# Optimization experiments

Measured on AMD Instinct MI355X. Metric: run time of the kernel, lower is better.

The kernel has to match this reference:

```python
import jax, jax.numpy as jnp
import numpy as np
import math

B, T, C, H = 4, 2048, 1024, 16
HS = C // H
EPS = 1e-5


def layernorm(x, g, b):
    mu = jnp.mean(x, axis=-1, keepdims=True)
    var = jnp.var(x, axis=-1, keepdims=True)
    return (x - mu) * jax.lax.rsqrt(var + EPS) * g + b


def setup_inputs() -> dict:
    key = jax.random.key(0)
    ks = jax.random.split(key, 7)
    rn = lambda k, s: jax.random.normal(k, s, dtype=jnp.float32) * 0.02
    return {
        "x": jax.random.normal(ks[0], (B, T, C), dtype=jnp.float32),
        "mask": jnp.tril(jnp.ones((T, T), dtype=jnp.int32)),  # causal tril buffer
        "wq": rn(ks[1], (H, HS, C)),  # stacked per-head Linear weights [out,in]
        "wk": rn(ks[2], (H, HS, C)),
        "wv": rn(ks[3], (H, HS, C)),
        "ln1_g": jnp.ones((C,), jnp.float32),
        "ln1_b": jnp.zeros((C,), jnp.float32),
        "ln2_g": jnp.ones((C,), jnp.float32),
        "ln2_b": jnp.zeros((C,), jnp.float32),
        "w1": rn(ks[4], (4 * C, C)),
        "b1": jnp.zeros((4 * C,), jnp.float32),
        "w2": rn(ks[5], (C, 4 * C)),
        "b2": jnp.zeros((C,), jnp.float32),
    }


def reference(x, mask, wq, wk, wv, ln1_g, ln1_b, ln2_g, ln2_b, w1, b1, w2, b2):
    Bx, Tx, Cx = x.shape
    h = layernorm(x, ln1_g, ln1_b)
    # per-head projections, batched over heads: [B,H,T,HS]
    q = jnp.einsum('btc,hdc->bhtd', h, wq)
    k = jnp.einsum('btc,hdc->bhtd', h, wk)
    v = jnp.einsum('btc,hdc->bhtd', h, wv)
    scores = jnp.einsum('bhtd,bhsd->bhts', q, k) * (1.0 / math.sqrt(HS))
    scores = jnp.where(mask[None, None, :Tx, :Tx] == 0, -jnp.inf, scores)
    w = jax.nn.softmax(scores, axis=-1)
    attn = jnp.einsum('bhts,bhsd->bhtd', w, v)  # [B,H,T,HS]
    attn = attn.transpose(0, 2, 1, 3).reshape(Bx, Tx, Cx)  # concat heads
    x = x + attn
    h2 = layernorm(x, ln2_g, ln2_b)
    ff = jax.nn.silu(h2 @ w1.T + b1) @ w2.T + b2  # dropout = identity (eval)
    return x + ff
```

## Files before the change

### kernel.cpp

```cpp
#include <hip/hip_runtime.h>
#include <stdint.h>

#define Bb 4
#define Tt 2048
#define Cc 1024
#define Hh 16
#define HSs 64

typedef __attribute__((ext_vector_type(8))) __bf16 bf16x8;
typedef __attribute__((ext_vector_type(4))) float f32x4;

__device__ __forceinline__ ushort f2bf(float f){
  union { float f; uint u; } c; c.f = f;
  return (ushort)((c.u + 0x8000u) >> 16);
}
__device__ __forceinline__ float bf2f(ushort u){
  union { uint u; float f; } c; c.u = ((uint)u) << 16; return c.f;
}

__device__ __forceinline__ void gload16(const void* g, void* l){
  __builtin_amdgcn_global_load_lds(
      (__attribute__((address_space(1))) void*)(g),
      (__attribute__((address_space(3))) void*)(l), 16, 0, 0);
}

__global__ __launch_bounds__(256) void cast_all_kernel(
    const float* __restrict__ wq, const float* __restrict__ wk,
    const float* __restrict__ wv, const float* __restrict__ w1,
    const float* __restrict__ w2, ushort* __restrict__ out){
  int i = (blockIdx.x * 256 + threadIdx.x) * 4;
  const float* src; int off;
  if      (i <  1048576){ src = wq; off = i; }
  else if (i <  2097152){ src = wk; off = i - 1048576; }
  else if (i <  3145728){ src = wv; off = i - 2097152; }
  else if (i <  7340032){ src = w1; off = i - 3145728; }
  else                  { src = w2; off = i - 7340032; }
  float4 v = *(const float4*)(src + off);
  ushort4 o; o.x = f2bf(v.x); o.y = f2bf(v.y); o.z = f2bf(v.z); o.w = f2bf(v.w);
  *(ushort4*)(out + i) = o;
}

__global__ __launch_bounds__(256) void add_p1_kernel(float* __restrict__ out,
                                                     const ushort* __restrict__ p1b){
  for (int it = 0; it < 4; ++it){
    size_t i = ((size_t)it * 2048 * 256 + blockIdx.x * 256 + threadIdx.x) * 4;
    float4 o = *(const float4*)(out + i);
    ushort4 p = *(const ushort4*)(p1b + i);
    o.x += bf2f(p.x); o.y += bf2f(p.y); o.z += bf2f(p.z); o.w += bf2f(p.w);
    *(float4*)(out + i) = o;
  }
}

__global__ __launch_bounds__(256) void ln1_kernel(const float* __restrict__ x,
    const float* __restrict__ gw, const float* __restrict__ bw,
    ushort* __restrict__ hout){
  int row = blockIdx.x, tid = threadIdx.x;
  size_t base = (size_t)row * Cc + tid * 4;
  float4 xv = *(const float4*)(x + base);
  float s  = xv.x + xv.y + xv.z + xv.w;
  float ss = xv.x*xv.x + xv.y*xv.y + xv.z*xv.z + xv.w*xv.w;
  #pragma unroll
  for (int off = 1; off < 64; off <<= 1){ s += __shfl_xor(s, off); ss += __shfl_xor(ss, off); }
  __shared__ float red[8];
  int wid = tid >> 6, lane = tid & 63;
  if (lane == 0){ red[wid] = s; red[4 + wid] = ss; }
  __syncthreads();
  s  = red[0] + red[1] + red[2] + red[3];
  ss = red[4] + red[5] + red[6] + red[7];
  float mu = s * (1.0f / Cc);
  float rstd = rsqrtf(ss * (1.0f / Cc) - mu * mu + 1e-5f);
  float4 gv = *(const float4*)(gw + tid * 4);
  float4 bv = *(const float4*)(bw + tid * 4);
  ushort4 o;
  o.x = f2bf((xv.x - mu) * rstd * gv.x + bv.x);
  o.y = f2bf((xv.y - mu) * rstd * gv.y + bv.y);
  o.z = f2bf((xv.z - mu) * rstd * gv.z + bv.z);
  o.w = f2bf((xv.w - mu) * rstd * gv.w + bv.w);
  *(ushort4*)(hout + base) = o;
}

__global__ __launch_bounds__(256) void ln2_kernel(const float* __restrict__ x,
    const ushort* __restrict__ attnb,
    const float* __restrict__ gw, const float* __restrict__ bw,
    float* __restrict__ x2, ushort* __restrict__ hout){
  int row = blockIdx.x, tid = threadIdx.x;
  size_t base = (size_t)row * Cc + tid * 4;
  float4 xv = *(const float4*)(x + base);
  ushort4 av = *(const ushort4*)(attnb + base);
  xv.x += bf2f(av.x); xv.y += bf2f(av.y); xv.z += bf2f(av.z); xv.w += bf2f(av.w);
  *(float4*)(x2 + base) = xv;
  float s  = xv.x + xv.y + xv.z + xv.w;
  float ss = xv.x*xv.x + xv.y*xv.y + xv.z*xv.z + xv.w*xv.w;
  #pragma unroll
  for (int off = 1; off < 64; off <<= 1){ s += __shfl_xor(s, off); ss += __shfl_xor(ss, off); }
  __shared__ float red[8];
  int wid = tid >> 6, lane = tid & 63;
  if (lane == 0){ red[wid] = s; red[4 + wid] = ss; }
  __syncthreads();
  s  = red[0] + red[1] + red[2] + red[3];
  ss = red[4] + red[5] + red[6] + red[7];
  float mu = s * (1.0f / Cc);
  float rstd = rsqrtf(ss * (1.0f / Cc) - mu * mu + 1e-5f);
  float4 gv = *(const float4*)(gw + tid * 4);
  float4 bv = *(const float4*)(bw + tid * 4);
  ushort4 o;
  o.x = f2bf((xv.x - mu) * rstd * gv.x + bv.x);
  o.y = f2bf((xv.y - mu) * rstd * gv.y + bv.y);
  o.z = f2bf((xv.z - mu) * rstd * gv.z + bv.z);
  o.w = f2bf((xv.w - mu) * rstd * gv.w + bv.w);
  *(ushort4*)(hout + base) = o;
}

#define MFMA_QUAD(SI, QI, BQ) \
  { \
    _Pragma("unroll") \
    for (int mi = 0; mi < 4; ++mi){ \
      acc[(SI)*4+mi][(QI)*2+0] = __builtin_amdgcn_mfma_f32_16x16x32_bf16(af[mi][0], BQ[0][0], acc[(SI)*4+mi][(QI)*2+0], 0,0,0); \
      acc[(SI)*4+mi][(QI)*2+0] = __builtin_amdgcn_mfma_f32_16x16x32_bf16(af[mi][1], BQ[0][1], acc[(SI)*4+mi][(QI)*2+0], 0,0,0); \
      acc[(SI)*4+mi][(QI)*2+1] = __builtin_amdgcn_mfma_f32_16x16x32_bf16(af[mi][0], BQ[1][0], acc[(SI)*4+mi][(QI)*2+1], 0,0,0); \
      acc[(SI)*4+mi][(QI)*2+1] = __builtin_amdgcn_mfma_f32_16x16x32_bf16(af[mi][1], BQ[1][1], acc[(SI)*4+mi][(QI)*2+1], 0,0,0); \
    } \
  }

#define PH_SYNC_PRE()  { __builtin_amdgcn_sched_barrier(0); __builtin_amdgcn_s_barrier(); \
                         asm volatile("s_waitcnt lgkmcnt(0)" ::: "memory"); \
                         __builtin_amdgcn_sched_barrier(0); __builtin_amdgcn_s_setprio(1); }
#define PH_SYNC_POST() { __builtin_amdgcn_s_setprio(0); __builtin_amdgcn_sched_barrier(0); \
                         __builtin_amdgcn_s_barrier(); }

template<int MODE>
__device__ __forceinline__ void gemm256_body(
    const ushort* __restrict__ A, const ushort* __restrict__ Bw,
    int N, int K, int ldO,
    ushort* __restrict__ obf, float* __restrict__ of32,
    ushort* __restrict__ p1b, const float* __restrict__ bias)
{
  __shared__ __align__(16) ushort lds[2][2][2][128 * 64];
  int tid = threadIdx.x, lane = tid & 63, wid = tid >> 6;
  int wm = wid >> 2, wn = wid & 3;
  int c = lane & 15, g = lane >> 4;

  int nwg = gridDim.x, bid = blockIdx.x;
  int wgid = (bid & 7) * (nwg >> 3) + (bid >> 3);
  int m0, n0, koff = 0;
  if (MODE == 3){
    int split = wgid >> 7, rem = wgid & 127;
    m0 = (rem >> 2) << 8; n0 = (rem & 3) << 8; koff = split << 11;
  } else {
    int nTn = N >> 8;
    m0 = (wgid / nTn) << 8; n0 = (wgid % nTn) << 8;
  }

  const ushort* Ag = A  + (size_t)m0 * K + koff;
  const ushort* Bg = Bw + (size_t)n0 * K + koff;

  auto stage = [&](const ushort* gbase, int t, int ab, int h){
    #pragma unroll
    for (int j = 0; j < 2; ++j){
      int d = j * 8192 + wid * 1024 + lane * 16;
      int row = d >> 7;
      int colb = (d & 127) ^ ((row & 7) << 4);
      gload16((const char*)gbase + ((size_t)(h * 128 + row) * K + t * 64) * 2 + colb,
              (char*)&lds[t & 1][ab][h][0] + j * 8192 + wid * 1024);
    }
  };

  f32x4 acc[8][4] = {};
  bf16x8 af[4][2], bq0[2][2], bq1[2][2];
  int nt = (MODE == 3) ? (K >> 7) : (K >> 6);

  stage(Ag, 0, 0, 0); stage(Ag, 0, 0, 1);
  stage(Bg, 0, 1, 0); stage(Bg, 0, 1, 1);
  stage(Bg, 1, 1, 0); stage(Bg, 1, 1, 1);
  asm volatile("s_waitcnt vmcnt(4)" ::: "memory");
  __builtin_amdgcn_sched_barrier(0);
  __builtin_amdgcn_s_barrier();

  for (int t = 0; t < nt; ++t){
    const char* Abuf = (const char*)&lds[t & 1][0][wm][0];
    const char* Bbuf = (const char*)&lds[t & 1][1][wn >> 1][0];
    int brow0 = (wn & 1) * 64;

    #pragma unroll
    for (int mi = 0; mi < 4; ++mi){
      int row = mi * 16 + c, sw = (row & 7) << 4;
      af[mi][0] = *(const bf16x8*)(Abuf + row * 128 + ((g * 16) ^ sw));
      af[mi][1] = *(const bf16x8*)(Abuf + row * 128 + ((64 + g * 16) ^ sw));
    }
    #pragma unroll
    for (int nj = 0; nj < 2; ++nj){
      int row = brow0 + nj * 16 + c, sw = (row & 7) << 4;
      bq0[nj][0] = *(const bf16x8*)(Bbuf + row * 128 + ((g * 16) ^ sw));
      bq0[nj][1] = *(const bf16x8*)(Bbuf + row * 128 + ((64 + g * 16) ^ sw));
    }
    if (t + 1 < nt) stage(Ag, t + 1, 0, 0);
    PH_SYNC_PRE();
    MFMA_QUAD(0, 0, bq0);
    PH_SYNC_POST();

    #pragma unroll
    for (int nj = 0; nj < 2; ++nj){
      int row = brow0 + 32 + nj * 16 + c, sw = (row & 7) << 4;
      bq1[nj][0] = *(const bf16x8*)(Bbuf + row * 128 + ((g * 16) ^ sw));
      bq1[nj][1] = *(const bf16x8*)(Bbuf + row * 128 + ((64 + g * 16) ^ sw));
    }
    if (t + 1 < nt) stage(Ag, t + 1, 0, 1);
    PH_SYNC_PRE();
    MFMA_QUAD(0, 1, bq1);
    PH_SYNC_POST();

    #pragma unroll
    for (int mi = 0; mi < 4; ++mi){
      int row = 64 + mi * 16 + c, sw = (row & 7) << 4;
      af[mi][0] = *(const bf16x8*)(Abuf + row * 128 + ((g * 16) ^ sw));
      af[mi][1] = *(const bf16x8*)(Abuf + row * 128 + ((64 + g * 16) ^ sw));
    }
    if (t + 2 < nt) stage(Bg, t + 2, 1, 0);
    PH_SYNC_PRE();
    MFMA_QUAD(1, 0, bq0);
    PH_SYNC_POST();

    if (t + 2 < nt){
      stage(Bg, t + 2, 1, 1);
      asm volatile("s_waitcnt vmcnt(4)" ::: "memory");
    } else {
      asm volatile("s_waitcnt vmcnt(0)" ::: "memory");
    }
    __builtin_amdgcn_sched_barrier(0);
    __builtin_amdgcn_s_barrier();
    __builtin_amdgcn_s_setprio(1);
    MFMA_QUAD(1, 1, bq1);
    PH_SYNC_POST();
  }

  #pragma unroll
  for (int mi = 0; mi < 8; ++mi){
    #pragma unroll
    for (int ni = 0; ni < 4; ++ni){
      #pragma unroll
      for (int r = 0; r < 4; ++r){
        float v = acc[mi][ni][r];
        int m = m0 + wm * 128 + mi * 16 + g * 4 + r;
        int n = n0 + wn * 64 + ni * 16 + c;
        if (MODE == 0){
          int which = n >> 10;
          int nn = n & 1023;
          int b = m >> 11, t = m & (Tt - 1);
          int h = nn >> 6, d = nn & 63;
          float vv = (which == 0) ? v * 0.125f : v;
          size_t base = (size_t)which * (size_t)(Bb * Tt * Cc);
          size_t idx = (which == 2)
              ? ((((size_t)(b * Hh + h)) * HSs + d) * Tt + t)
              : ((((size_t)(b * Hh + h)) * Tt + t) * HSs + d);
          obf[base + idx] = f2bf(vv);
        } else if (MODE == 1){
          v += bias[n];
          float sv = v / (1.0f + __expf(-v));
          obf[(size_t)m * ldO + n] = f2bf(sv);
        } else {
          size_t idx = (size_t)m * N + n;
          if (koff == 0) of32[idx] = of32[idx] + v + bias[n];
          else           p1b[idx] = f2bf(v);
        }
      }
    }
  }
}

__global__ __launch_bounds__(512, 2) void gemm_qkv_kernel(
    const ushort* __restrict__ A, const ushort* __restrict__ Bw, int N, int K,
    ushort* __restrict__ obf){
  gemm256_body<0>(A, Bw, N, K, 0, obf, nullptr, nullptr, nullptr);
}
__global__ __launch_bounds__(512, 2) void gemm_ffn1_kernel(
    const ushort* __restrict__ A, const ushort* __restrict__ Bw, int N, int K, int ldO,
    ushort* __restrict__ obf, const float* __restrict__ bias){
  gemm256_body<1>(A, Bw, N, K, ldO, obf, nullptr, nullptr, bias);
}
__global__ __launch_bounds__(512, 2) void gemm_ffn2_kernel(
    const ushort* __restrict__ A, const ushort* __restrict__ Bw, int N, int K,
    float* __restrict__ of32, ushort* __restrict__ p1b, const float* __restrict__ bias){
  gemm256_body<3>(A, Bw, N, K, N, nullptr, of32, p1b, bias);
}

__global__ __launch_bounds__(256, 2) void attn_kernel(
    const ushort* __restrict__ q, const ushort* __restrict__ k,
    const ushort* __restrict__ vt, ushort* __restrict__ attnb)
{
  __shared__ __align__(16) ushort Ksm[4][64 * 64];
  __shared__ __align__(16) ushort Vsm[4][64 * 64];
  __shared__ __align__(16) ushort Pl[4][32 * 64];

  int bh  = blockIdx.y;
  int p   = blockIdx.x;
  int tid = threadIdx.x, wid = tid >> 6, lane = tid & 63;
  int g = lane >> 4, c = lane & 15;
  int qbA = 15 - p, qbB = p;
  int q0A = qbA * 128 + wid * 32;
  int q0B = qbB * 128 + wid * 32;
  const ushort* Qb = q  + (size_t)bh * Tt * HSs;
  const ushort* Kb = k  + (size_t)bh * Tt * HSs;
  const ushort* Vt = vt + (size_t)bh * HSs * Tt;
  char* Pw = (char*)&Pl[wid][0];

  auto stageKV = [&](int bsel, int s0){
    #pragma unroll
    for (int half = 0; half < 2; ++half){
      int i = wid + half * 4;
      int row = i * 8 + (lane >> 3);
      int col = ((lane & 7) ^ (row & 7)) * 8;
      gload16(Kb + (size_t)(s0 + row) * HSs + col, &Ksm[bsel][i * 512]);
      gload16(Vt + (size_t)row * Tt + s0 + col,    &Vsm[bsel][i * 512]);
    }
  };

  bf16x8 qfA[2][2], qfB[2][2];
  #pragma unroll
  for (int mi = 0; mi < 2; ++mi)
    #pragma unroll
    for (int ks = 0; ks < 2; ++ks){
      qfA[mi][ks] = *(const bf16x8*)(Qb + (size_t)(q0A + mi * 16 + c) * HSs + ks * 32 + g * 8);
      qfB[mi][ks] = *(const bf16x8*)(Qb + (size_t)(q0B + mi * 16 + c) * HSs + ks * 32 + g * 8);
    }

  f32x4 oA[2][4] = {}, oB[2][4] = {};
  float mA[2][4], lA[2][4], mB[2][4], lB[2][4];
  #pragma unroll
  for (int mi = 0; mi < 2; ++mi)
    #pragma unroll
    for (int r = 0; r < 4; ++r){
      mA[mi][r] = -1e30f; lA[mi][r] = 0.f;
      mB[mi][r] = -1e30f; lB[mi][r] = 0.f;
    }

  auto computeTile = [&](bf16x8 (&qf)[2][2], f32x4 (&o)[2][4],
                         float (&mrow)[2][4], float (&lpart)[2][4],
                         int q0w, int s0, const char* Kbuf, const char* Vbuf){
    f32x4 S[2][4] = {};
    bf16x8 kf[4][2];
    #pragma unroll
    for (int ni = 0; ni < 4; ++ni)
      #pragma unroll
      for (int ks = 0; ks < 2; ++ks)
        kf[ni][ks] = *(const bf16x8*)(Kbuf + (ni * 16 + c) * 128 + (((ks * 4 + g) ^ (c & 7)) << 4));
    #pragma unroll
    for (int mi = 0; mi < 2; ++mi)
      #pragma unroll
      for (int ni = 0; ni < 4; ++ni)
        #pragma unroll
        for (int ks = 0; ks < 2; ++ks)
          S[mi][ni] = __builtin_amdgcn_mfma_f32_16x16x32_bf16(qf[mi][ks], kf[ni][ks], S[mi][ni], 0, 0, 0);

    if (s0 + 63 > q0w){
      #pragma unroll
      for (int mi = 0; mi < 2; ++mi)
        #pragma unroll
        for (int ni = 0; ni < 4; ++ni)
          #pragma unroll
          for (int r = 0; r < 4; ++r){
            int tl = q0w + mi * 16 + g * 4 + r, sl = s0 + ni * 16 + c;
            if (sl > tl) S[mi][ni][r] = -1e30f;
          }
    }

    float lmax[2][4], worst = -1e30f;
    #pragma unroll
    for (int mi = 0; mi < 2; ++mi)
      #pragma unroll
      for (int r = 0; r < 4; ++r){
        float a0 = fmaxf(S[mi][0][r], S[mi][1][r]);
        float a1 = fmaxf(S[mi][2][r], S[mi][3][r]);
        lmax[mi][r] = fmaxf(a0, a1);
        worst = fmaxf(worst, lmax[mi][r] - mrow[mi][r]);
      }
    if (!__all(worst <= 8.0f)){
      #pragma unroll
      for (int mi = 0; mi < 2; ++mi)
        #pragma unroll
        for (int r = 0; r < 4; ++r){
          float mx = lmax[mi][r];
          mx = fmaxf(mx, __shfl_xor(mx, 1));
          mx = fmaxf(mx, __shfl_xor(mx, 2));
          mx = fmaxf(mx, __shfl_xor(mx, 4));
          mx = fmaxf(mx, __shfl_xor(mx, 8));
          float mnew  = fmaxf(mrow[mi][r], mx);
          float alpha = __expf(mrow[mi][r] - mnew);
          lpart[mi][r] *= alpha;
          #pragma unroll
          for (int dt = 0; dt < 4; ++dt) o[mi][dt][r] *= alpha;
          mrow[mi][r] = mnew;
        }
    }
    #pragma unroll
    for (int mi = 0; mi < 2; ++mi)
      #pragma unroll
      for (int r = 0; r < 4; ++r){
        int row = mi * 16 + g * 4 + r;
        float mb = mrow[mi][r] * 1.44269504f;
        float pp[4];
        #pragma unroll
        for (int ni = 0; ni < 4; ++ni){
          pp[ni] = exp2f(__builtin_fmaf(S[mi][ni][r], 1.44269504f, -mb));
          *(ushort*)(Pw + row * 128 + (((ni * 32 + 2 * c) ^ ((row & 7) << 4)))) = f2bf(pp[ni]);
        }
        lpart[mi][r] += (pp[0] + pp[1]) + (pp[2] + pp[3]);
      }

    bf16x8 vf[4][2];
    #pragma unroll
    for (int dt = 0; dt < 4; ++dt)
      #pragma unroll
      for (int ks = 0; ks < 2; ++ks)
        vf[dt][ks] = *(const bf16x8*)(Vbuf + (dt * 16 + c) * 128 + (((ks * 4 + g) ^ (c & 7)) << 4));
    #pragma unroll
    for (int mi = 0; mi < 2; ++mi){
      #pragma unroll
      for (int ks = 0; ks < 2; ++ks){
        bf16x8 pf = *(const bf16x8*)(Pw + (mi * 16 + c) * 128 + ((((ks * 4 + g) ^ (c & 7)) << 4)));
        #pragma unroll
        for (int dt = 0; dt < 4; ++dt)
          o[mi][dt] = __builtin_amdgcn_mfma_f32_16x16x32_bf16(pf, vf[dt][ks], o[mi][dt], 0, 0, 0);
      }
    }
  };

  int nchA = 2 * qbA + 2;

  stageKV(0, 0);
  stageKV(1, 64);

  for (int ch = 0; ch < nchA; ch += 2){
    bool staged = (ch + 2 < nchA);
    if (staged){
      stageKV((ch + 2) & 3, (ch + 2) * 64);
      stageKV((ch + 3) & 3, (ch + 3) * 64);
      asm volatile("s_waitcnt vmcnt(8)" ::: "memory");
    } else {
      asm volatile("s_waitcnt vmcnt(0)" ::: "memory");
    }
    __builtin_amdgcn_sched_barrier(0);
    __builtin_amdgcn_s_barrier();

    {
      int s0 = ch * 64;
      const char* Kbuf = (const char*)&Ksm[ch & 3][0];
      const char* Vbuf = (const char*)&Vsm[ch & 3][0];
      if (s0 <= q0A + 31) computeTile(qfA, oA, mA, lA, q0A, s0, Kbuf, Vbuf);
      if (s0 <= q0B + 31) computeTile(qfB, oB, mB, lB, q0B, s0, Kbuf, Vbuf);
    }
    {
      int s0 = (ch + 1) * 64;
      const char* Kbuf = (const char*)&Ksm[(ch + 1) & 3][0];
      const char* Vbuf = (const char*)&Vsm[(ch + 1) & 3][0];
      if (s0 <= q0A + 31) computeTile(qfA, oA, mA, lA, q0A, s0, Kbuf, Vbuf);
      if (s0 <= q0B + 31) computeTile(qfB, oB, mB, lB, q0B, s0, Kbuf, Vbuf);
    }

    __builtin_amdgcn_sched_barrier(0);
    __builtin_amdgcn_s_barrier();
  }

  int b = bh >> 4, h = bh & 15;
  #pragma unroll
  for (int mi = 0; mi < 2; ++mi)
    #pragma unroll
    for (int r = 0; r < 4; ++r){
      float la = lA[mi][r];
      la += __shfl_xor(la, 1); la += __shfl_xor(la, 2);
      la += __shfl_xor(la, 4); la += __shfl_xor(la, 8);
      float lia = 1.0f / la;
      float lb = lB[mi][r];
      lb += __shfl_xor(lb, 1); lb += __shfl_xor(lb, 2);
      lb += __shfl_xor(lb, 4); lb += __shfl_xor(lb, 8);
      float lib = 1.0f / lb;
      #pragma unroll
      for (int dt = 0; dt < 4; ++dt){
        int tA = q0A + mi * 16 + g * 4 + r;
        int tB = q0B + mi * 16 + g * 4 + r;
        attnb[((size_t)(b * Tt + tA)) * Cc + h * HSs + dt * 16 + c] = f2bf(oA[mi][dt][r] * lia);
        attnb[((size_t)(b * Tt + tB)) * Cc + h * HSs + dt * 16 + c] = f2bf(oB[mi][dt][r] * lib);
      }
    }
}

extern "C" void kernel_launch(void* const* d_in, const int* in_sizes, int n_in,
                              void* d_out, int out_size, void* d_ws, size_t ws_size,
                              hipStream_t stream) {
  (void)in_sizes; (void)n_in; (void)out_size; (void)ws_size;
  const float* x    = (const float*)d_in[0];
  const float* wq   = (const float*)d_in[2];
  const float* wk   = (const float*)d_in[3];
  const float* wv   = (const float*)d_in[4];
  const float* ln1g = (const float*)d_in[5];
  const float* ln1b = (const float*)d_in[6];
  const float* ln2g = (const float*)d_in[7];
  const float* ln2b = (const float*)d_in[8];
  const float* w1   = (const float*)d_in[9];
  const float* b1   = (const float*)d_in[10];
  const float* w2   = (const float*)d_in[11];
  const float* b2   = (const float*)d_in[12];
  float* out = (float*)d_out;

  char* ws = (char*)d_ws;
  const size_t SZ_ACT = (size_t)Bb * Tt * Cc * 2;
  ushort* h1    = (ushort*)(ws);
  ushort* qbuf  = (ushort*)(ws + SZ_ACT);
  ushort* kbuf  = (ushort*)(ws + 2 * SZ_ACT);
  ushort* vbuf  = (ushort*)(ws + 3 * SZ_ACT);
  ushort* attnb = (ushort*)(ws + 4 * SZ_ACT);
  ushort* h2    = (ushort*)(ws + 5 * SZ_ACT);
  ushort* h3    = (ushort*)(ws + 6 * SZ_ACT);
  ushort* p1b   = (ushort*)(ws + SZ_ACT);
  char*   wsw   = ws + 6 * SZ_ACT + (size_t)Bb * Tt * 4 * Cc * 2;
  ushort* wqb = (ushort*)(wsw);
  ushort* w1b = (ushort*)(wsw + 3 * (size_t)Cc * Cc * 2);
  ushort* w2b = (ushort*)(wsw + 3 * (size_t)Cc * Cc * 2 + (size_t)4 * Cc * Cc * 2);

  cast_all_kernel<<<dim3(11264), 256, 0, stream>>>(wq, wk, wv, w1, w2, wqb);

  ln1_kernel<<<dim3(Bb * Tt), 256, 0, stream>>>(x, ln1g, ln1b, h1);

  gemm_qkv_kernel<<<dim3(32 * 12), 512, 0, stream>>>(h1, wqb, 3 * Cc, Cc, qbuf);

  attn_kernel<<<dim3(8, Bb * Hh), 256, 0, stream>>>(qbuf, kbuf, vbuf, attnb);

  ln2_kernel<<<dim3(Bb * Tt), 256, 0, stream>>>(x, attnb, ln2g, ln2b, out, h2);

  gemm_ffn1_kernel<<<dim3(32 * 8), 512, 0, stream>>>(h2, w1b,                      2048, Cc, 4 * Cc, h3,        b1);
  gemm_ffn1_kernel<<<dim3(32 * 8), 512, 0, stream>>>(h2, w1b + (size_t)2048 * Cc,  2048, Cc, 4 * Cc, h3 + 2048, b1 + 2048);
  gemm_ffn2_kernel<<<dim3(256), 512, 0, stream>>>(h3, w2b, Cc, 4 * Cc, out, p1b, b2);
  add_p1_kernel<<<dim3(2048), 256, 0, stream>>>(out, p1b);
}
```

Measured before the change: 401.1 us.

## Software-pipeline GEMM LDS reads behind MFMA phases with prefetched fragments

Restructures the 256x256 GEMM main loop so each phase issues MFMAs on fragments already in registers, then reads the next phase's A/B fragments from LDS. The first fragments of the next K-tile are loaded at the end of the current one. A-tile global loads are issued two iterations ahead, like the B tiles. The aim is to hide LDS read latency and cut one barrier per phase, at the cost of extra registers (double A fragments) and more delicate vmcnt accounting.

```diff
diff --git a/kernel.cpp b/kernel.cpp
--- a/kernel.cpp
+++ b/kernel.cpp
@@ -111,22 +111,21 @@
   *(ushort4*)(hout + base) = o;
 }
 
-#define MFMA_QUAD(SI, QI, BQ) \
+#define MFMA_QUAD(AF, SI, QI, BQ) \
   { \
     _Pragma("unroll") \
     for (int mi = 0; mi < 4; ++mi){ \
-      acc[(SI)*4+mi][(QI)*2+0] = __builtin_amdgcn_mfma_f32_16x16x32_bf16(af[mi][0], BQ[0][0], acc[(SI)*4+mi][(QI)*2+0], 0,0,0); \
-      acc[(SI)*4+mi][(QI)*2+0] = __builtin_amdgcn_mfma_f32_16x16x32_bf16(af[mi][1], BQ[0][1], acc[(SI)*4+mi][(QI)*2+0], 0,0,0); \
-      acc[(SI)*4+mi][(QI)*2+1] = __builtin_amdgcn_mfma_f32_16x16x32_bf16(af[mi][0], BQ[1][0], acc[(SI)*4+mi][(QI)*2+1], 0,0,0); \
-      acc[(SI)*4+mi][(QI)*2+1] = __builtin_amdgcn_mfma_f32_16x16x32_bf16(af[mi][1], BQ[1][1], acc[(SI)*4+mi][(QI)*2+1], 0,0,0); \
+      acc[(SI)*4+mi][(QI)*2+0] = __builtin_amdgcn_mfma_f32_16x16x32_bf16(AF[mi][0], BQ[0][0], acc[(SI)*4+mi][(QI)*2+0], 0,0,0); \
+      acc[(SI)*4+mi][(QI)*2+0] = __builtin_amdgcn_mfma_f32_16x16x32_bf16(AF[mi][1], BQ[0][1], acc[(SI)*4+mi][(QI)*2+0], 0,0,0); \
+      acc[(SI)*4+mi][(QI)*2+1] = __builtin_amdgcn_mfma_f32_16x16x32_bf16(AF[mi][0], BQ[1][0], acc[(SI)*4+mi][(QI)*2+1], 0,0,0); \
+      acc[(SI)*4+mi][(QI)*2+1] = __builtin_amdgcn_mfma_f32_16x16x32_bf16(AF[mi][1], BQ[1][1], acc[(SI)*4+mi][(QI)*2+1], 0,0,0); \
     } \
   }
 
-#define PH_SYNC_PRE()  { __builtin_amdgcn_sched_barrier(0); __builtin_amdgcn_s_barrier(); \
-                         asm volatile("s_waitcnt lgkmcnt(0)" ::: "memory"); \
-                         __builtin_amdgcn_sched_barrier(0); __builtin_amdgcn_s_setprio(1); }
-#define PH_SYNC_POST() { __builtin_amdgcn_s_setprio(0); __builtin_amdgcn_sched_barrier(0); \
-                         __builtin_amdgcn_s_barrier(); }
+#define GEMM_TOP() { asm volatile("s_waitcnt lgkmcnt(0)" ::: "memory"); \
+                     __builtin_amdgcn_sched_barrier(0); __builtin_amdgcn_s_setprio(1); }
+#define GEMM_MID() { __builtin_amdgcn_s_setprio(0); }
+#define GEMM_BAR() { __builtin_amdgcn_s_barrier(); }
 
 template<int MODE>
 __device__ __forceinline__ void gemm256_body(
@@ -139,6 +138,7 @@
   int tid = threadIdx.x, lane = tid & 63, wid = tid >> 6;
   int wm = wid >> 2, wn = wid & 3;
   int c = lane & 15, g = lane >> 4;
+  int brow0 = (wn & 1) * 64;
 
   int nwg = gridDim.x, bid = blockIdx.x;
   int wgid = (bid & 7) * (nwg >> 3) + (bid >> 3);
@@ -154,83 +154,94 @@
   const ushort* Ag = A  + (size_t)m0 * K + koff;
   const ushort* Bg = Bw + (size_t)n0 * K + koff;
 
-  auto stage = [&](const ushort* gbase, int t, int ab, int h){
+  auto stage = [&](const ushort* gbase, int t, int ab, int hb){
     #pragma unroll
     for (int j = 0; j < 2; ++j){
       int d = j * 8192 + wid * 1024 + lane * 16;
       int row = d >> 7;
       int colb = (d & 127) ^ ((row & 7) << 4);
-      gload16((const char*)gbase + ((size_t)(h * 128 + row) * K + t * 64) * 2 + colb,
-              (char*)&lds[t & 1][ab][h][0] + j * 8192 + wid * 1024);
+      gload16((const char*)gbase + ((size_t)(hb * 128 + row) * K + t * 64) * 2 + colb,
+              (char*)&lds[t & 1][ab][hb][0] + j * 8192 + wid * 1024);
     }
   };
 
   f32x4 acc[8][4] = {};
-  bf16x8 af[4][2], bq0[2][2], bq1[2][2];
+  bf16x8 af0[4][2], af1[4][2], bq0[2][2], bq1[2][2];
+
+  auto readA = [&](const char* Ap, int sub, bf16x8 (&af)[4][2]){
+    #pragma unroll
+    for (int mi = 0; mi < 4; ++mi){
+      int row = sub * 64 + mi * 16 + c, sw = (row & 7) << 4;
+      af[mi][0] = *(const bf16x8*)(Ap + row * 128 + ((g * 16) ^ sw));
+      af[mi][1] = *(const bf16x8*)(Ap + row * 128 + ((64 + g * 16) ^ sw));
+    }
+  };
+  auto readB = [&](const char* Bp, int hb, bf16x8 (&bq)[2][2]){
+    #pragma unroll
+    for (int nj = 0; nj < 2; ++nj){
+      int row = brow0 + hb * 32 + nj * 16 + c, sw = (row & 7) << 4;
+      bq[nj][0] = *(const bf16x8*)(Bp + row * 128 + ((g * 16) ^ sw));
+      bq[nj][1] = *(const bf16x8*)(Bp + row * 128 + ((64 + g * 16) ^ sw));
+    }
+  };
+
   int nt = (MODE == 3) ? (K >> 7) : (K >> 6);
 
   stage(Ag, 0, 0, 0); stage(Ag, 0, 0, 1);
   stage(Bg, 0, 1, 0); stage(Bg, 0, 1, 1);
-  stage(Bg, 1, 1, 0); stage(Bg, 1, 1, 1);
-  asm volatile("s_waitcnt vmcnt(4)" ::: "memory");
-  __builtin_amdgcn_sched_barrier(0);
+  if (nt > 1){
+    stage(Bg, 1, 1, 0); stage(Bg, 1, 1, 1);
+    stage(Ag, 1, 0, 0); stage(Ag, 1, 0, 1);
+    asm volatile("s_waitcnt vmcnt(8)" ::: "memory");
+  } else {
+    asm volatile("s_waitcnt vmcnt(0)" ::: "memory");
+  }
   __builtin_amdgcn_s_barrier();
+  readA((const char*)&lds[0][0][wm][0], 0, af0);
+  readB((const char*)&lds[0][1][wn >> 1][0], 0, bq0);
 
   for (int t = 0; t < nt; ++t){
-    const char* Abuf = (const char*)&lds[t & 1][0][wm][0];
-    const char* Bbuf = (const char*)&lds[t & 1][1][wn >> 1][0];
-    int brow0 = (wn & 1) * 64;
-
-    #pragma unroll
-    for (int mi = 0; mi < 4; ++mi){
-      int row = mi * 16 + c, sw = (row & 7) << 4;
-      af[mi][0] = *(const bf16x8*)(Abuf + row * 128 + ((g * 16) ^ sw));
-      af[mi][1] = *(const bf16x8*)(Abuf + row * 128 + ((64 + g * 16) ^ sw));
-    }
-    #pragma unroll
-    for (int nj = 0; nj < 2; ++nj){
-      int row = brow0 + nj * 16 + c, sw = (row & 7) << 4;
-      bq0[nj][0] = *(const bf16x8*)(Bbuf + row * 128 + ((g * 16) ^ sw));
-      bq0[nj][1] = *(const bf16x8*)(Bbuf + row * 128 + ((64 + g * 16) ^ sw));
-    }
-    if (t + 1 < nt) stage(Ag, t + 1, 0, 0);
-    PH_SYNC_PRE();
-    MFMA_QUAD(0, 0, bq0);
-    PH_SYNC_POST();
-
-    #pragma unroll
-    for (int nj = 0; nj < 2; ++nj){
-      int row = brow0 + 32 + nj * 16 + c, sw = (row & 7) << 4;
-      bq1[nj][0] = *(const bf16x8*)(Bbuf + row * 128 + ((g * 16) ^ sw));
-      bq1[nj][1] = *(const bf16x8*)(Bbuf + row * 128 + ((64 + g * 16) ^ sw));
-    }
-    if (t + 1 < nt) stage(Ag, t + 1, 0, 1);
-    PH_SYNC_PRE();
-    MFMA_QUAD(0, 1, bq1);
-    PH_SYNC_POST();
-
-    #pragma unroll
-    for (int mi = 0; mi < 4; ++mi){
-      int row = 64 + mi * 16 + c, sw = (row & 7) << 4;
-      af[mi][0] = *(const bf16x8*)(Abuf + row * 128 + ((g * 16) ^ sw));
-      af[mi][1] = *(const bf16x8*)(Abuf + row * 128 + ((64 + g * 16) ^ sw));
-    }
-    if (t + 2 < nt) stage(Bg, t + 2, 1, 0);
-    PH_SYNC_PRE();
-    MFMA_QUAD(1, 0, bq0);
-    PH_SYNC_POST();
-
+    const char* Abuf  = (const char*)&lds[t & 1][0][wm][0];
+    const char* Bbuf  = (const char*)&lds[t & 1][1][wn >> 1][0];
+    const char* AbufN = (const char*)&lds[(t + 1) & 1][0][wm][0];
+    const char* BbufN = (const char*)&lds[(t + 1) & 1][1][wn >> 1][0];
+
+    GEMM_TOP();
+    MFMA_QUAD(af0, 0, 0, bq0);
+    GEMM_MID();
+    readB(Bbuf, 1, bq1);
+    GEMM_BAR();
+
+    GEMM_TOP();
+    MFMA_QUAD(af0, 0, 1, bq1);
+    GEMM_MID();
+    readA(Abuf, 1, af1);
+    GEMM_BAR();
+
+    GEMM_TOP();
+    MFMA_QUAD(af1, 1, 0, bq0);
+    GEMM_MID();
+    if (t + 2 < nt){
+      stage(Bg, t + 2, 1, 0);
+      asm volatile("s_waitcnt vmcnt(2)" ::: "memory");
+    } else {
+      asm volatile("s_waitcnt vmcnt(0)" ::: "memory");
+    }
+    GEMM_BAR();
+
+    GEMM_TOP();
+    MFMA_QUAD(af1, 1, 1, bq1);
+    GEMM_MID();
+    if (t + 1 < nt){
+      readA(AbufN, 0, af0);
+      readB(BbufN, 0, bq0);
+    }
     if (t + 2 < nt){
       stage(Bg, t + 2, 1, 1);
-      asm volatile("s_waitcnt vmcnt(4)" ::: "memory");
-    } else {
-      asm volatile("s_waitcnt vmcnt(0)" ::: "memory");
-    }
-    __builtin_amdgcn_sched_barrier(0);
-    __builtin_amdgcn_s_barrier();
-    __builtin_amdgcn_s_setprio(1);
-    MFMA_QUAD(1, 1, bq1);
-    PH_SYNC_POST();
+      stage(Ag, t + 2, 0, 0);
+      stage(Ag, t + 2, 0, 1);
+    }
+    GEMM_BAR();
   }
 
   #pragma unroll
@@ -305,8 +316,8 @@
 
   auto stageKV = [&](int bsel, int s0){
     #pragma unroll
-    for (int half = 0; half < 2; ++half){
-      int i = wid + half * 4;
+    for (int hb = 0; hb < 2; ++hb){
+      int i = wid + hb * 4;
       int row = i * 8 + (lane >> 3);
       int col = ((lane & 7) ^ (row & 7)) * 8;
       gload16(Kb + (size_t)(s0 + row) * HSs + col, &Ksm[bsel][i * 512]);
```

Measured after the change: 395.1 us. Within noise of the previous version (-1.5%).

## Rewrite GEMM to 128x256 tiles with triple-buffered K=32 stages

Applied to the files above, without the earlier changes.

Replaces the 256x256 GEMM tile, which used a K=64 double buffer and four barrier-separated MFMA phases, with a 128x256 tile. The new loop uses K=32 steps, a three-slot LDS ring that prefetches two steps ahead, and a single MFMA block per iteration. Smaller tiles and fewer accumulators allow launch_bounds occupancy of 4 and double the grid sizes, aiming to fill the CUs better and cut sync overhead. The trade-off is less data reuse per tile and a barrier on every short K step. K is now a template constant.

```diff
diff --git a/kernel.cpp b/kernel.cpp
--- a/kernel.cpp
+++ b/kernel.cpp
@@ -111,31 +111,15 @@
   *(ushort4*)(hout + base) = o;
 }
 
-#define MFMA_QUAD(SI, QI, BQ) \
-  { \
-    _Pragma("unroll") \
-    for (int mi = 0; mi < 4; ++mi){ \
-      acc[(SI)*4+mi][(QI)*2+0] = __builtin_amdgcn_mfma_f32_16x16x32_bf16(af[mi][0], BQ[0][0], acc[(SI)*4+mi][(QI)*2+0], 0,0,0); \
-      acc[(SI)*4+mi][(QI)*2+0] = __builtin_amdgcn_mfma_f32_16x16x32_bf16(af[mi][1], BQ[0][1], acc[(SI)*4+mi][(QI)*2+0], 0,0,0); \
-      acc[(SI)*4+mi][(QI)*2+1] = __builtin_amdgcn_mfma_f32_16x16x32_bf16(af[mi][0], BQ[1][0], acc[(SI)*4+mi][(QI)*2+1], 0,0,0); \
-      acc[(SI)*4+mi][(QI)*2+1] = __builtin_amdgcn_mfma_f32_16x16x32_bf16(af[mi][1], BQ[1][1], acc[(SI)*4+mi][(QI)*2+1], 0,0,0); \
-    } \
-  }
-
-#define PH_SYNC_PRE()  { __builtin_amdgcn_sched_barrier(0); __builtin_amdgcn_s_barrier(); \
-                         asm volatile("s_waitcnt lgkmcnt(0)" ::: "memory"); \
-                         __builtin_amdgcn_sched_barrier(0); __builtin_amdgcn_s_setprio(1); }
-#define PH_SYNC_POST() { __builtin_amdgcn_s_setprio(0); __builtin_amdgcn_sched_barrier(0); \
-                         __builtin_amdgcn_s_barrier(); }
-
-template<int MODE>
-__device__ __forceinline__ void gemm256_body(
+template<int MODE, int KV>
+__device__ __forceinline__ void gemm_body(
     const ushort* __restrict__ A, const ushort* __restrict__ Bw,
-    int N, int K, int ldO,
+    int N, int ldO,
     ushort* __restrict__ obf, float* __restrict__ of32,
     ushort* __restrict__ p1b, const float* __restrict__ bias)
 {
-  __shared__ __align__(16) ushort lds[2][2][2][128 * 64];
+  __shared__ __align__(16) ushort ldsA[3][128 * 32];
+  __shared__ __align__(16) ushort ldsB[3][256 * 32];
   int tid = threadIdx.x, lane = tid & 63, wid = tid >> 6;
   int wm = wid >> 2, wn = wid & 3;
   int c = lane & 15, g = lane >> 4;
@@ -144,114 +128,106 @@
   int wgid = (bid & 7) * (nwg >> 3) + (bid >> 3);
   int m0, n0, koff = 0;
   if (MODE == 3){
-    int split = wgid >> 7, rem = wgid & 127;
-    m0 = (rem >> 2) << 8; n0 = (rem & 3) << 8; koff = split << 11;
+    int split = wgid >> 8, rem = wgid & 255;
+    m0 = (rem >> 2) << 7; n0 = (rem & 3) << 8; koff = split << 11;
   } else {
     int nTn = N >> 8;
-    m0 = (wgid / nTn) << 8; n0 = (wgid % nTn) << 8;
+    m0 = (wgid / nTn) << 7; n0 = (wgid % nTn) << 8;
   }
-
-  const ushort* Ag = A  + (size_t)m0 * K + koff;
-  const ushort* Bg = Bw + (size_t)n0 * K + koff;
-
-  auto stage = [&](const ushort* gbase, int t, int ab, int h){
+  int nt = (MODE == 3) ? 64 : (KV >> 5);
+
+  const ushort* Ag = A  + (size_t)m0 * KV + koff;
+  const ushort* Bg = Bw + (size_t)n0 * KV + koff;
+
+  auto stageA = [&](int t, int bsel){
+    int d = wid * 1024 + lane * 16;
+    int row = d >> 6, cs = (d >> 4) & 3;
+    int ce = (cs ^ ((row >> 1) & 3)) * 8;
+    gload16(Ag + (size_t)row * KV + t * 32 + ce,
+            (char*)&ldsA[bsel][0] + wid * 1024);
+  };
+  auto stageB = [&](int t, int bsel){
     #pragma unroll
     for (int j = 0; j < 2; ++j){
       int d = j * 8192 + wid * 1024 + lane * 16;
-      int row = d >> 7;
-      int colb = (d & 127) ^ ((row & 7) << 4);
-      gload16((const char*)gbase + ((size_t)(h * 128 + row) * K + t * 64) * 2 + colb,
-              (char*)&lds[t & 1][ab][h][0] + j * 8192 + wid * 1024);
+      int row = d >> 6, cs = (d >> 4) & 3;
+      int ce = (cs ^ ((row >> 1) & 3)) * 8;
+      gload16(Bg + (size_t)row * KV + t * 32 + ce,
+              (char*)&ldsB[bsel][0] + j * 8192 + wid * 1024);
     }
   };
 
-  f32x4 acc[8][4] = {};
-  bf16x8 af[4][2], bq0[2][2], bq1[2][2];
-  int nt = (MODE == 3) ? (K >> 7) : (K >> 6);
-
-  stage(Ag, 0, 0, 0); stage(Ag, 0, 0, 1);
-  stage(Bg, 0, 1, 0); stage(Bg, 0, 1, 1);
-  stage(Bg, 1, 1, 0); stage(Bg, 1, 1, 1);
-  asm volatile("s_waitcnt vmcnt(4)" ::: "memory");
-  __builtin_amdgcn_sched_barrier(0);
+  f32x4 acc[4][4] = {};
+  bf16x8 af[4], bq[4];
+
+  auto readFrags = [&](int bsel){
+    const char* Ap = (const char*)&ldsA[bsel][0];
+    const char* Bp = (const char*)&ldsB[bsel][0];
+    #pragma unroll
+    for (int mi = 0; mi < 4; ++mi){
+      int row = wm * 64 + mi * 16 + c;
+      af[mi] = *(const bf16x8*)(Ap + row * 64 + ((g * 16) ^ (((row >> 1) & 3) << 4)));
+    }
+    #pragma unroll
+    for (int ni = 0; ni < 4; ++ni){
+      int row = wn * 64 + ni * 16 + c;
+      bq[ni] = *(const bf16x8*)(Bp + row * 64 + ((g * 16) ^ (((row >> 1) & 3) << 4)));
+    }
+  };
+
+  stageA(0, 0); stageB(0, 0);
+  stageA(1, 1); stageB(1, 1);
+  asm volatile("s_waitcnt vmcnt(3)" ::: "memory");
   __builtin_amdgcn_s_barrier();
-
+  readFrags(0);
+
+  int bc = 0;
   for (int t = 0; t < nt; ++t){
-    const char* Abuf = (const char*)&lds[t & 1][0][wm][0];
-    const char* Bbuf = (const char*)&lds[t & 1][1][wn >> 1][0];
-    int brow0 = (wn & 1) * 64;
-
-    #pragma unroll
-    for (int mi = 0; mi < 4; ++mi){
-      int row = mi * 16 + c, sw = (row & 7) << 4;
-      af[mi][0] = *(const bf16x8*)(Abuf + row * 128 + ((g * 16) ^ sw));
-      af[mi][1] = *(const bf16x8*)(Abuf + row * 128 + ((64 + g * 16) ^ sw));
-    }
-    #pragma unroll
-    for (int nj = 0; nj < 2; ++nj){
-      int row = brow0 + nj * 16 + c, sw = (row & 7) << 4;
-      bq0[nj][0] = *(const bf16x8*)(Bbuf + row * 128 + ((g * 16) ^ sw));
-      bq0[nj][1] = *(const bf16x8*)(Bbuf + row * 128 + ((64 + g * 16) ^ sw));
-    }
-    if (t + 1 < nt) stage(Ag, t + 1, 0, 0);
-    PH_SYNC_PRE();
-    MFMA_QUAD(0, 0, bq0);
-    PH_SYNC_POST();
-
-    #pragma unroll
-    for (int nj = 0; nj < 2; ++nj){
-      int row = brow0 + 32 + nj * 16 + c, sw = (row & 7) << 4;
-      bq1[nj][0] = *(const bf16x8*)(Bbuf + row * 128 + ((g * 16) ^ sw));
-      bq1[nj][1] = *(const bf16x8*)(Bbuf + row * 128 + ((64 + g * 16) ^ sw));
-    }
-    if (t + 1 < nt) stage(Ag, t + 1, 0, 1);
-    PH_SYNC_PRE();
-    MFMA_QUAD(0, 1, bq1);
-    PH_SYNC_POST();
-
-    #pragma unroll
-    for (int mi = 0; mi < 4; ++mi){
-      int row = 64 + mi * 16 + c, sw = (row & 7) << 4;
-      af[mi][0] = *(const bf16x8*)(Abuf + row * 128 + ((g * 16) ^ sw));
-      af[mi][1] = *(const bf16x8*)(Abuf + row * 128 + ((64 + g * 16) ^ sw));
-    }
-    if (t + 2 < nt) stage(Bg, t + 2, 1, 0);
-    PH_SYNC_PRE();
-    MFMA_QUAD(1, 0, bq0);
-    PH_SYNC_POST();
-
+    asm volatile("s_waitcnt lgkmcnt(0)" ::: "memory");
+    __builtin_amdgcn_sched_barrier(0);
+    __builtin_amdgcn_s_setprio(1);
+    #pragma unroll
+    for (int mi = 0; mi < 4; ++mi)
+      #pragma unroll
+      for (int ni = 0; ni < 4; ++ni)
+        acc[mi][ni] = __builtin_amdgcn_mfma_f32_16x16x32_bf16(af[mi], bq[ni], acc[mi][ni], 0, 0, 0);
+    __builtin_amdgcn_s_setprio(0);
+    __builtin_amdgcn_sched_barrier(0);
+
+    int bs = (bc == 0) ? 2 : bc - 1;
     if (t + 2 < nt){
-      stage(Bg, t + 2, 1, 1);
-      asm volatile("s_waitcnt vmcnt(4)" ::: "memory");
+      stageA(t + 2, bs); stageB(t + 2, bs);
+      asm volatile("s_waitcnt vmcnt(3)" ::: "memory");
     } else {
       asm volatile("s_waitcnt vmcnt(0)" ::: "memory");
     }
     __builtin_amdgcn_sched_barrier(0);
     __builtin_amdgcn_s_barrier();
-    __builtin_amdgcn_s_setprio(1);
-    MFMA_QUAD(1, 1, bq1);
-    PH_SYNC_POST();
+
+    int bn = (bc == 2) ? 0 : bc + 1;
+    if (t + 1 < nt) readFrags(bn);
+    bc = bn;
   }
 
   #pragma unroll
-  for (int mi = 0; mi < 8; ++mi){
+  for (int mi = 0; mi < 4; ++mi){
     #pragma unroll
     for (int ni = 0; ni < 4; ++ni){
       #pragma unroll
       for (int r = 0; r < 4; ++r){
         float v = acc[mi][ni][r];
-        int m = m0 + wm * 128 + mi * 16 + g * 4 + r;
+        int m = m0 + wm * 64 + mi * 16 + g * 4 + r;
         int n = n0 + wn * 64 + ni * 16 + c;
         if (MODE == 0){
           int which = n >> 10;
           int nn = n & 1023;
-          int b = m >> 11, t = m & (Tt - 1);
+          int b = m >> 11, ti = m & (Tt - 1);
           int h = nn >> 6, d = nn & 63;
           float vv = (which == 0) ? v * 0.125f : v;
           size_t base = (size_t)which * (size_t)(Bb * Tt * Cc);
           size_t idx = (which == 2)
-              ? ((((size_t)(b * Hh + h)) * HSs + d) * Tt + t)
-              : ((((size_t)(b * Hh + h)) * Tt + t) * HSs + d);
+              ? ((((size_t)(b * Hh + h)) * HSs + d) * Tt + ti)
+              : ((((size_t)(b * Hh + h)) * Tt + ti) * HSs + d);
           obf[base + idx] = f2bf(vv);
         } else if (MODE == 1){
           v += bias[n];
@@ -267,20 +243,20 @@
   }
 }
 
-__global__ __launch_bounds__(512, 2) void gemm_qkv_kernel(
-    const ushort* __restrict__ A, const ushort* __restrict__ Bw, int N, int K,
+__global__ __launch_bounds__(512, 4) void gemm_qkv_kernel(
+    const ushort* __restrict__ A, const ushort* __restrict__ Bw, int N,
     ushort* __restrict__ obf){
-  gemm256_body<0>(A, Bw, N, K, 0, obf, nullptr, nullptr, nullptr);
-}
-__global__ __launch_bounds__(512, 2) void gemm_ffn1_kernel(
-    const ushort* __restrict__ A, const ushort* __restrict__ Bw, int N, int K, int ldO,
+  gemm_body<0, 1024>(A, Bw, N, 0, obf, nullptr, nullptr, nullptr);
+}
+__global__ __launch_bounds__(512, 4) void gemm_ffn1_kernel(
+    const ushort* __restrict__ A, const ushort* __restrict__ Bw, int N, int ldO,
     ushort* __restrict__ obf, const float* __restrict__ bias){
-  gemm256_body<1>(A, Bw, N, K, ldO, obf, nullptr, nullptr, bias);
-}
-__global__ __launch_bounds__(512, 2) void gemm_ffn2_kernel(
-    const ushort* __restrict__ A, const ushort* __restrict__ Bw, int N, int K,
+  gemm_body<1, 1024>(A, Bw, N, ldO, obf, nullptr, nullptr, bias);
+}
+__global__ __launch_bounds__(512, 4) void gemm_ffn2_kernel(
+    const ushort* __restrict__ A, const ushort* __restrict__ Bw, int N,
     float* __restrict__ of32, ushort* __restrict__ p1b, const float* __restrict__ bias){
-  gemm256_body<3>(A, Bw, N, K, N, nullptr, of32, p1b, bias);
+  gemm_body<3, 4096>(A, Bw, N, N, nullptr, of32, p1b, bias);
 }
 
 __global__ __launch_bounds__(256, 2) void attn_kernel(
@@ -305,8 +281,8 @@
 
   auto stageKV = [&](int bsel, int s0){
     #pragma unroll
-    for (int half = 0; half < 2; ++half){
-      int i = wid + half * 4;
+    for (int hb = 0; hb < 2; ++hb){
+      int i = wid + hb * 4;
       int row = i * 8 + (lane >> 3);
       int col = ((lane & 7) ^ (row & 7)) * 8;
       gload16(Kb + (size_t)(s0 + row) * HSs + col, &Ksm[bsel][i * 512]);
@@ -520,14 +496,14 @@
 
   ln1_kernel<<<dim3(Bb * Tt), 256, 0, stream>>>(x, ln1g, ln1b, h1);
 
-  gemm_qkv_kernel<<<dim3(32 * 12), 512, 0, stream>>>(h1, wqb, 3 * Cc, Cc, qbuf);
+  gemm_qkv_kernel<<<dim3(768), 512, 0, stream>>>(h1, wqb, 3 * Cc, qbuf);
 
   attn_kernel<<<dim3(8, Bb * Hh), 256, 0, stream>>>(qbuf, kbuf, vbuf, attnb);
 
   ln2_kernel<<<dim3(Bb * Tt), 256, 0, stream>>>(x, attnb, ln2g, ln2b, out, h2);
 
-  gemm_ffn1_kernel<<<dim3(32 * 8), 512, 0, stream>>>(h2, w1b,                      2048, Cc, 4 * Cc, h3,        b1);
-  gemm_ffn1_kernel<<<dim3(32 * 8), 512, 0, stream>>>(h2, w1b + (size_t)2048 * Cc,  2048, Cc, 4 * Cc, h3 + 2048, b1 + 2048);
-  gemm_ffn2_kernel<<<dim3(256), 512, 0, stream>>>(h3, w2b, Cc, 4 * Cc, out, p1b, b2);
+  gemm_ffn1_kernel<<<dim3(512), 512, 0, stream>>>(h2, w1b,                     2048, 4 * Cc, h3,        b1);
+  gemm_ffn1_kernel<<<dim3(512), 512, 0, stream>>>(h2, w1b + (size_t)2048 * Cc, 2048, 4 * Cc, h3 + 2048, b1 + 2048);
+  gemm_ffn2_kernel<<<dim3(512), 512, 0, stream>>>(h3, w2b, Cc, out, p1b, b2);
   add_p1_kernel<<<dim3(2048), 256, 0, stream>>>(out, p1b);
 }
```

Result: slower. 421.8 us (+5.2%).
